# Kernel optimization log

Hardware: AMD Instinct MI355X
Metric: run time of the kernel (lower is better)

The kernel has to match this reference:

```python
import jax, jax.numpy as jnp
import numpy as np

N = 100000   # nodes
E = 1250000  # edges
IN, HID, OUT = 64, 128, 32


def _gcn_norm(edge_index, num_nodes):
    # add self loops, unit edge weights, symmetric normalization (PyG gcn_norm)
    loops = jnp.arange(num_nodes, dtype=edge_index.dtype)
    src = jnp.concatenate([edge_index[0], loops])
    dst = jnp.concatenate([edge_index[1], loops])
    w = jnp.ones(src.shape[0], dtype=jnp.float32)
    deg = jax.ops.segment_sum(w, dst, num_segments=num_nodes)  # degree at targets
    dis = jnp.where(deg > 0, jax.lax.rsqrt(deg), 0.0)
    norm = dis[src] * dis[dst]  # per-edge coefficient
    return src, dst, norm


def _gcn_conv(h, W, b, src, dst, norm, num_nodes):
    hw = h @ W                                 # [N, out] linear transform first
    msg = hw[src] * norm[:, None]              # gather + scale  [E+N, out]
    agg = jax.ops.segment_sum(msg, dst, num_segments=num_nodes)
    return agg + b


def setup_inputs() -> dict:
    key = jax.random.key(0)
    ks = jax.random.split(key, 8)
    x = jax.random.normal(ks[0], (N, IN), dtype=jnp.float32)
    edge_index = jax.random.randint(ks[1], (2, E), 0, N, dtype=jnp.int32)
    def glorot(k, fan_in, fan_out):
        s = np.sqrt(6.0 / (fan_in + fan_out)).astype(np.float32)
        return jax.random.uniform(k, (fan_in, fan_out), jnp.float32, -s, s)
    return {
        "x": x,
        "edge_index": edge_index,
        "W1": glorot(ks[2], IN, HID),   "b1": jnp.zeros((HID,), jnp.float32),
        "W_mu": glorot(ks[3], HID, OUT), "b_mu": jnp.zeros((OUT,), jnp.float32),
        "W_lv": glorot(ks[4], HID, OUT), "b_lv": jnp.zeros((OUT,), jnp.float32),
    }


def reference(x, edge_index, W1, b1, W_mu, b_mu, W_lv, b_lv):
    src, dst, norm = _gcn_norm(edge_index, N)
    h = _gcn_conv(x, W1, b1, src, dst, norm, N)
    h = jax.nn.selu(h)
    # dropout: eval mode (training=False) -> identity
    mu = _gcn_conv(h, W_mu, b_mu, src, dst, norm, N)
    logvar = _gcn_conv(h, W_lv, b_lv, src, dst, norm, N)
    return (mu, logvar)
```

## Files before the change

kernel.cpp:

```cpp
#include <hip/hip_runtime.h>
#include <math.h>

#define NN 100000
#define NE 1250000
#define DIN 64
#define DHID 128
#define DO2 64
#define DOUT 32

#define NBIN 256
#define BINW ((NN + NBIN - 1) / NBIN)
#define NSEG 153
#define C2 80
#define PADESRC 10944
#define P1_THREADS 1024
#define P1_EPT 8
#define P1_EPB (P1_THREADS * P1_EPT)

typedef unsigned int uint;
typedef unsigned short ushort;
typedef __attribute__((ext_vector_type(8))) short bf16x8;
typedef __attribute__((ext_vector_type(4))) float f32x4;

#define MFMA16(A, B, C) __builtin_amdgcn_mfma_f32_16x16x32_bf16(A, B, C, 0, 0, 0)

__device__ __forceinline__ ushort f2bf(float f) {
    uint u = __float_as_uint(f);
    uint r = (u + 0x7fffu + ((u >> 16) & 1u)) >> 16;
    return (ushort)r;
}
__device__ __forceinline__ uint pack2(float a, float b) {
    return (uint)f2bf(a) | ((uint)f2bf(b) << 16);
}
__device__ __forceinline__ float bflo(uint p) { return __uint_as_float(p << 16); }
__device__ __forceinline__ float bfhi(uint p) { return __uint_as_float(p & 0xffff0000u); }

__device__ __forceinline__ int nofk(int k) {
    return (k & 3) | (((k >> 3) & 3) << 2) | (((k >> 2) & 1) << 4) | ((k >> 5) << 5);
}

#define ACC8(A, P) do { \
    A##0 += bflo((P).x); A##1 += bfhi((P).x); \
    A##2 += bflo((P).y); A##3 += bfhi((P).y); \
    A##4 += bflo((P).z); A##5 += bfhi((P).z); \
    A##6 += bflo((P).w); A##7 += bfhi((P).w); } while (0)

__global__ __launch_bounds__(P1_THREADS) void scatter_direct(const int* __restrict__ src,
                                                             const int* __restrict__ dst,
                                                             uint* __restrict__ ebin,
                                                             int* __restrict__ cnt, int n) {
    __shared__ int hist[NBIN];
    int tid = threadIdx.x;
    if (tid < NBIN) hist[tid] = 0;
    __syncthreads();
    int bi = blockIdx.x;
    int base = bi * P1_EPB;
#pragma unroll
    for (int j = 0; j < P1_EPT; j++) {
        int i = base + j * P1_THREADS + tid;
        if (i < n) {
            int d = dst[i];
            int bb = d / BINW;
            uint e = ((uint)src[i] << 9) | (uint)(d - bb * BINW);
            int rk = atomicAdd(&hist[bb], 1);
            if (rk < C2) ebin[((size_t)bb * NSEG + bi) * C2 + rk] = e;
        }
    }
    __syncthreads();
    if (tid < NBIN) cnt[tid * NSEG + bi] = min(hist[tid], C2);
}

__global__ __launch_bounds__(512) void finalize_prep(const uint* __restrict__ ebin,
                                                     const int* __restrict__ cnt,
                                                     const float* __restrict__ x,
                                                     const float* __restrict__ W1,
                                                     const float* __restrict__ Wmu,
                                                     const float* __restrict__ Wlv,
                                                     float* __restrict__ dis,
                                                     int2* __restrict__ prange,
                                                     int* __restrict__ esrc,
                                                     uint* __restrict__ xb,
                                                     ushort* __restrict__ Wall) {
    __shared__ int hh[BINW];
    __shared__ int base_s[BINW];
    __shared__ int cur_s[BINW];
    __shared__ float dd[BINW];
    int b = blockIdx.x;
    int tid = threadIdx.x;
    int v0 = b * BINW;
    int nv = min(BINW, NN - v0);
    int pbase = PADESRC * b;
    for (int i = tid; i < BINW; i += 512) { hh[i] = 0; cur_s[i] = 0; }
    __syncthreads();
    int wv = tid >> 6, ln = tid & 63;
    for (int s = wv; s < NSEG; s += 8) {
        int m = cnt[b * NSEG + s];
        const uint* cell = ebin + ((size_t)b * NSEG + s) * C2;
        for (int j = ln; j < m; j += 64)
            atomicAdd(&hh[cell[j] & 511u], 1);
    }
    __syncthreads();
    int c = (tid < nv) ? hh[tid] : 0;
    int p = (c + 7) & ~7;
    __syncthreads();
    if (tid < nv) hh[tid] = p;
    __syncthreads();
    for (int off = 1; off < BINW; off <<= 1) {
        int t = (tid < nv && tid >= off) ? hh[tid - off] : 0;
        __syncthreads();
        if (tid < nv) hh[tid] += t;
        __syncthreads();
    }
    if (tid < nv) {
        int base = pbase + hh[tid] - p;
        base_s[tid] = base;
        prange[v0 + tid] = make_int2(base, base + p);
        float dv = rsqrtf((float)c + 1.0f);
        dis[v0 + tid] = dv;
        dd[tid] = dv;
        for (int j = c; j < p; j++) esrc[base + j] = NN;
    }
    __syncthreads();
    for (int s = wv; s < NSEG; s += 8) {
        int m = cnt[b * NSEG + s];
        const uint* cell = ebin + ((size_t)b * NSEG + s) * C2;
        for (int j = ln; j < m; j += 64) {
            uint e = cell[j];
            int l = (int)(e & 511u);
            int pos = base_s[l] + atomicAdd(&cur_s[l], 1);
            esrc[pos] = (int)(e >> 9);
        }
    }
    for (int idx = tid; idx < nv * 8; idx += 512) {
        int r = idx >> 3, q = idx & 7;
        float dv = dd[r];
        int row = v0 + r;
        const float4* xs = (const float4*)(x + (size_t)row * 64 + q * 8);
        float4 u0 = xs[0], u1 = xs[1];
        uint4 o;
        o.x = pack2(dv * u0.x, dv * u0.y);
        o.y = pack2(dv * u0.z, dv * u0.w);
        o.z = pack2(dv * u1.x, dv * u1.y);
        o.w = pack2(dv * u1.z, dv * u1.w);
        *(uint4*)(xb + (size_t)row * 32 + q * 4) = o;
    }
    if (b == NBIN - 1 && tid < 32) xb[(size_t)NN * 32 + tid] = 0;
    if (tid < 64) {
        int i = b * 64 + tid;
        if (i < 8192) {
            int lane = (i >> 3) & 63, e = i & 7;
            int fr = i >> 9;
            int t = fr >> 1, ks = fr & 1;
            int row = 16 * t + (lane & 15);
            int k = ks * 32 + (lane >> 4) * 8 + e;
            float w = W1[k * DHID + row];
            ushort hi = f2bf(w);
            Wall[i] = hi;
            Wall[8192 + i] = f2bf(w - bflo((uint)hi));
        } else {
            int ii = i - 8192;
            int lane = (ii >> 3) & 63, e = ii & 7;
            int fr = ii >> 9;
            int t2 = fr >> 2, ks = fr & 3;
            int nout = 16 * t2 + (lane & 15);
            int kpos = ks * 32 + (lane >> 4) * 8 + e;
            int h = nofk(kpos);
            float w = (nout < DOUT) ? Wmu[h * DOUT + nout] : Wlv[h * DOUT + (nout - DOUT)];
            ushort hi = f2bf(w);
            Wall[16384 + ii] = hi;
            Wall[24576 + ii] = f2bf(w - bflo((uint)hi));
        }
    }
}

#define GATHER_CORE(TBL)                                                            \
    int tid = threadIdx.x;                                                          \
    int lane = tid & 63;                                                            \
    int sub = lane & 15;                                                            \
    int epar = sub >> 3;                                                            \
    int f4 = (sub & 7) * 4;                                                         \
    int nlb = lane & 48;                                                            \
    int v = blockIdx.x * 16 + (tid >> 4);                 \
    int2 rng = prange[v];                                                           \
    int beg = rng.x, nb = rng.y - rng.x;                      \
    uint4 pv = *(const uint4*)(TBL + (size_t)v * 32 + f4);                          \
    float dv = dis[v];                                                              \
    int sreg  = esrc[beg + sub];                                                    \
    int sreg2 = esrc[beg + 16 + sub];                     \
    int svals[16];                                                                  \
    _Pragma("unroll")                                                               \
    for (int it = 0; it < 4; it++) {                                                \
        svals[2 * it]     = __shfl(sreg,  nlb | (epar + 4 * it));                   \
        svals[2 * it + 1] = __shfl(sreg,  nlb | (epar + 4 * it + 2));               \
    }                                                                               \
    _Pragma("unroll")                                                               \
    for (int it = 4; it < 8; it++) {                                                \
        svals[2 * it]     = __shfl(sreg2, nlb | (epar + 4 * it - 16));              \
        svals[2 * it + 1] = __shfl(sreg2, nlb | (epar + 4 * it - 14));              \
    }                                                                               \
    float a0 = 0.f, a1 = 0.f, a2 = 0.f, a3 = 0.f, a4 = 0.f, a5 = 0.f, a6 = 0.f, a7 = 0.f; \
    float b0 = 0.f, b1 = 0.f, b2 = 0.f, b3 = 0.f, b4 = 0.f, b5 = 0.f, b6 = 0.f, b7 = 0.f; \
    int lim = nb < 32 ? nb : 32;                                                    \
    int nit = lim >> 2;                                                             \
    _Pragma("unroll")                                                               \
    for (int it = 0; it < 4; it++) {                                                \
        int s0 = (it < nit) ? svals[2 * it]     : NN;                               \
        int s1 = (it < nit) ? svals[2 * it + 1] : NN;                               \
        uint4 pA = *(const uint4*)(TBL + (size_t)s0 * 32 + f4);                     \
        uint4 pB = *(const uint4*)(TBL + (size_t)s1 * 32 + f4);                     \
        ACC8(a, pA); ACC8(b, pB);                                                   \
    }                                                                               \
    if (__any(nit > 4)) {                                                           \
        _Pragma("unroll")                                                           \
        for (int it = 4; it < 8; it++) {                                            \
            int s0 = (it < nit) ? svals[2 * it]     : NN;                           \
            int s1 = (it < nit) ? svals[2 * it + 1] : NN;                           \
            uint4 pA = *(const uint4*)(TBL + (size_t)s0 * 32 + f4);                 \
            uint4 pB = *(const uint4*)(TBL + (size_t)s1 * 32 + f4);                 \
            ACC8(a, pA); ACC8(b, pB);                                               \
        }                                                                           \
    }                                                                               \
    if (__any(nb > 32)) {                                                           \
        for (int idx = 32 + epar; idx < nb; idx += 2) {      \
            int s = esrc[beg + idx];                                                \
            uint4 p = *(const uint4*)(TBL + (size_t)s * 32 + f4);                   \
            ACC8(b, p);                                                             \
        }                                                                           \
    }                                                                               \
    a0 += b0; a1 += b1; a2 += b2; a3 += b3; a4 += b4; a5 += b5; a6 += b6; a7 += b7; \
    a0 += __shfl_xor(a0, 8); a1 += __shfl_xor(a1, 8);                               \
    a2 += __shfl_xor(a2, 8); a3 += __shfl_xor(a3, 8);                               \
    a4 += __shfl_xor(a4, 8); a5 += __shfl_xor(a5, 8);                               \
    a6 += __shfl_xor(a6, 8); a7 += __shfl_xor(a7, 8);                               \
    ACC8(a, pv);

__global__ __launch_bounds__(256) void aggregateX(const uint* __restrict__ xsb,
                                                  const int2* __restrict__ prange,
                                                  const int* __restrict__ esrc,
                                                  const float* __restrict__ dis,
                                                  uint* __restrict__ axb) {
    GATHER_CORE(xsb)
    if (!epar) {
        uint4 o;
        o.x = pack2(dv * a0, dv * a1);
        o.y = pack2(dv * a2, dv * a3);
        o.z = pack2(dv * a4, dv * a5);
        o.w = pack2(dv * a6, dv * a7);
        *(uint4*)(axb + (size_t)v * 32 + f4) = o;
    }
}

__device__ __forceinline__ float selu_f(float v) {
    const float scale = 1.0507009873554805f;
    const float alpha = 1.6732632423543772f;
    return scale * (v > 0.f ? v : alpha * (expf(v) - 1.f));
}

__global__ __launch_bounds__(256) void gemm_fused(const uint* __restrict__ axb,
                                                  const ushort* __restrict__ Wall,
                                                  const float* __restrict__ b1,
                                                  const float* __restrict__ dis,
                                                  uint* __restrict__ hw2s) {
    __shared__ ushort Wlds[32768];
    int tid = threadIdx.x;
    int lane = tid & 63;
    int xr = lane & 15, q = lane >> 4;
    int rowbase = blockIdx.x * 128 + (tid >> 6) * 16;
    int v0 = rowbase + xr;
    int v1 = rowbase + 64 + xr;
    int v0c = min(v0, NN - 1);
    int v1c = min(v1, NN - 1);

    bf16x8 bf0[2], bf1[2];
#pragma unroll
    for (int ks = 0; ks < 2; ks++) {
        bf0[ks] = *(const bf16x8*)(axb + (size_t)v0c * 32 + ks * 16 + q * 4);
        bf1[ks] = *(const bf16x8*)(axb + (size_t)v1c * 32 + ks * 16 + q * 4);
    }

    {
        const uint4* wsrc = (const uint4*)Wall;
        uint4* wdst = (uint4*)Wlds;
#pragma unroll
        for (int c = 0; c < 16; c++) wdst[tid + c * 256] = wsrc[tid + c * 256];
    }
    __syncthreads();

    const char* ldsb = (const char*)Wlds;
    int lane16 = lane * 16;

    uint px0[8], py0[8], px1[8], py1[8];
#pragma unroll
    for (int t = 0; t < 8; t++) {
        bf16x8 ah0 = *(const bf16x8*)(ldsb + (t * 2 + 0) * 1024 + lane16);
        bf16x8 ah1 = *(const bf16x8*)(ldsb + (t * 2 + 1) * 1024 + lane16);
        bf16x8 al0 = *(const bf16x8*)(ldsb + 16384 + (t * 2 + 0) * 1024 + lane16);
        bf16x8 al1 = *(const bf16x8*)(ldsb + 16384 + (t * 2 + 1) * 1024 + lane16);
        f32x4 acc0 = {0.f, 0.f, 0.f, 0.f};
        f32x4 acc1 = {0.f, 0.f, 0.f, 0.f};
        acc0 = MFMA16(ah0, bf0[0], acc0); acc0 = MFMA16(al0, bf0[0], acc0);
        acc0 = MFMA16(ah1, bf0[1], acc0); acc0 = MFMA16(al1, bf0[1], acc0);
        acc1 = MFMA16(ah0, bf1[0], acc1); acc1 = MFMA16(al0, bf1[0], acc1);
        acc1 = MFMA16(ah1, bf1[1], acc1); acc1 = MFMA16(al1, bf1[1], acc1);
        float4 bb = *(const float4*)(b1 + 16 * t + 4 * q);
        px0[t] = pack2(selu_f(acc0[0] + bb.x), selu_f(acc0[1] + bb.y));
        py0[t] = pack2(selu_f(acc0[2] + bb.z), selu_f(acc0[3] + bb.w));
        px1[t] = pack2(selu_f(acc1[0] + bb.x), selu_f(acc1[1] + bb.y));
        py1[t] = pack2(selu_f(acc1[2] + bb.z), selu_f(acc1[3] + bb.w));
    }

    float dv0 = dis[v0c], dv1 = dis[v1c];
#pragma unroll
    for (int t2 = 0; t2 < 4; t2++) {
        f32x4 a0 = {0.f, 0.f, 0.f, 0.f};
        f32x4 a1 = {0.f, 0.f, 0.f, 0.f};
#pragma unroll
        for (int ks = 0; ks < 4; ks++) {
            bf16x8 ah = *(const bf16x8*)(ldsb + 32768 + (t2 * 4 + ks) * 1024 + lane16);
            bf16x8 al = *(const bf16x8*)(ldsb + 49152 + (t2 * 4 + ks) * 1024 + lane16);
            bf16x8 fr0, fr1;
            *(uint4*)&fr0 = make_uint4(px0[2 * ks], py0[2 * ks], px0[2 * ks + 1], py0[2 * ks + 1]);
            *(uint4*)&fr1 = make_uint4(px1[2 * ks], py1[2 * ks], px1[2 * ks + 1], py1[2 * ks + 1]);
            a0 = MFMA16(ah, fr0, a0); a0 = MFMA16(al, fr0, a0);
            a1 = MFMA16(ah, fr1, a1); a1 = MFMA16(al, fr1, a1);
        }
        if (v0 < NN) {
            uint2 pk;
            pk.x = pack2(dv0 * a0[0], dv0 * a0[1]);
            pk.y = pack2(dv0 * a0[2], dv0 * a0[3]);
            *(uint2*)(hw2s + (size_t)v0 * 32 + t2 * 8 + q * 2) = pk;
        }
        if (v1 < NN) {
            uint2 pk;
            pk.x = pack2(dv1 * a1[0], dv1 * a1[1]);
            pk.y = pack2(dv1 * a1[2], dv1 * a1[3]);
            *(uint2*)(hw2s + (size_t)v1 * 32 + t2 * 8 + q * 2) = pk;
        }
    }
}

__global__ __launch_bounds__(256) void aggregate2(const uint* __restrict__ hw2s,
                                                  const int2* __restrict__ prange,
                                                  const int* __restrict__ esrc,
                                                  const float* __restrict__ dis,
                                                  const float* __restrict__ bmu,
                                                  const float* __restrict__ blv,
                                                  float* __restrict__ out) {
    GATHER_CORE(hw2s)
    if (!epar) {
        int j = sub & 7;
        const float* bp = (j < 4) ? (bmu + 8 * j) : (blv + 8 * j - 32);
        float* op = (j < 4) ? (out + (size_t)v * DOUT + 8 * j)
                            : (out + (size_t)NN * DOUT + (size_t)v * DOUT + 8 * j - 32);
        float4 c0 = *(const float4*)bp;
        float4 c1 = *(const float4*)(bp + 4);
        *(float4*)op       = make_float4(dv * a0 + c0.x, dv * a1 + c0.y,
                                         dv * a2 + c0.z, dv * a3 + c0.w);
        *(float4*)(op + 4) = make_float4(dv * a4 + c1.x, dv * a5 + c1.y,
                                         dv * a6 + c1.z, dv * a7 + c1.w);
    }
}

extern "C" void kernel_launch(void* const* d_in, const int* in_sizes, int n_in,
                              void* d_out, int out_size, void* d_ws, size_t ws_size,
                              hipStream_t stream) {
    const float* x   = (const float*)d_in[0];
    const int*   ei  = (const int*)d_in[1];
    const int*   e_src = ei;
    const int*   e_dst = ei + NE;
    const float* W1  = (const float*)d_in[2];
    const float* b1  = (const float*)d_in[3];
    const float* Wmu = (const float*)d_in[4];
    const float* bmu = (const float*)d_in[5];
    const float* Wlv = (const float*)d_in[6];
    const float* blv = (const float*)d_in[7];
    float* out = (float*)d_out;

    char* ws = (char*)d_ws;
    size_t off = 0;
    auto alloc = [&](size_t bytes) -> void* {
        void* p = ws + off;
        off += (bytes + 255) & ~(size_t)255;
        return p;
    };
    int2*   prange    = (int2*)alloc((size_t)NN * 8);
    int*    esrc      = (int*)alloc(((size_t)NBIN * PADESRC + 64) * 4);
    int*    cnt       = (int*)alloc((size_t)NBIN * NSEG * 4);
    float*  dis       = (float*)alloc((size_t)NN * 4);
    ushort* Wall      = (ushort*)alloc((size_t)32768 * 2);
    uint*   xb        = (uint*)alloc((size_t)(NN + 1) * 32 * 4);
    uint*   axb       = (uint*)alloc((size_t)NN * 32 * 4);
    uint*   hw2s      = xb;
    uint*   ebin      = axb;

    scatter_direct<<<NSEG, P1_THREADS, 0, stream>>>(e_src, e_dst, ebin, cnt, NE);
    finalize_prep<<<NBIN, 512, 0, stream>>>(ebin, cnt, x, W1, Wmu, Wlv,
                                            dis, prange, esrc, xb, Wall);
    aggregateX<<<NN / 16, 256, 0, stream>>>(xb, prange, esrc, dis, axb);
    gemm_fused<<<(NN + 127) / 128, 256, 0, stream>>>(axb, Wall, b1, dis, hw2s);
    aggregate2<<<NN / 16, 256, 0, stream>>>(hw2s, prange, esrc, dis, bmu, blv, out);
}
```

Baseline: 203.0 us.

## Split node feature tables into four column planes to shrink gather footprint

Bf16 feature tables (xb, axb, hw2s) are stored as four column-plane arrays of 16 features per node instead of one 64-wide row. The gather kernels launch four times as many blocks, one plane per block group, with 8 edge lanes times 2 feature quarters per node. The aim is a smaller per-pass working set so random neighbor gathers hit cache better. In exchange, prange, esrc and neighbor indices are re-read four times, and the per-node reduction needs more shuffles.

```diff
diff --git a/kernel.cpp b/kernel.cpp
--- a/kernel.cpp
+++ b/kernel.cpp
@@ -16,6 +16,7 @@
 #define P1_THREADS 1024
 #define P1_EPT 8
 #define P1_EPB (P1_THREADS * P1_EPT)
+#define NVB 6250
 
 typedef unsigned int uint;
 typedef unsigned short ushort;
@@ -142,9 +143,10 @@
         o.y = pack2(dv * u0.z, dv * u0.w);
         o.z = pack2(dv * u1.x, dv * u1.y);
         o.w = pack2(dv * u1.z, dv * u1.w);
-        *(uint4*)(xb + (size_t)row * 32 + q * 4) = o;
-    }
-    if (b == NBIN - 1 && tid < 32) xb[(size_t)NN * 32 + tid] = 0;
+        *(uint4*)(xb + ((size_t)(q >> 1) * (NN + 1) + row) * 8 + (q & 1) * 4) = o;
+    }
+    if (b == NBIN - 1 && tid < 32)
+        xb[((size_t)(tid >> 3) * (NN + 1) + NN) * 8 + (tid & 7)] = 0;
     if (tid < 64) {
         int i = b * 64 + tid;
         if (i < 8192) {
@@ -173,65 +175,59 @@
     }
 }
 
-#define GATHER_CORE(TBL)                                                            \
+#define GATHER_CORE_P(TBL)                                                          \
     int tid = threadIdx.x;                                                          \
     int lane = tid & 63;                                                            \
     int sub = lane & 15;                                                            \
-    int epar = sub >> 3;                                                            \
-    int f4 = (sub & 7) * 4;                                                         \
+    int fl4 = (sub & 1) * 4;                                                        \
+    int es  = sub >> 1;                                                             \
     int nlb = lane & 48;                                                            \
-    int v = blockIdx.x * 16 + (tid >> 4);                 \
+    int pb = blockIdx.x / NVB;                                                      \
+    int vb = blockIdx.x - pb * NVB;                                                 \
+    int v = vb * 16 + (tid >> 4);                          \
+    const uint* tb = (TBL) + (size_t)pb * (NN + 1) * 8;                             \
     int2 rng = prange[v];                                                           \
     int beg = rng.x, nb = rng.y - rng.x;                      \
-    uint4 pv = *(const uint4*)(TBL + (size_t)v * 32 + f4);                          \
+    uint4 pv = *(const uint4*)(tb + (size_t)v * 8 + fl4);                           \
     float dv = dis[v];                                                              \
     int sreg  = esrc[beg + sub];                                                    \
     int sreg2 = esrc[beg + 16 + sub];                     \
-    int svals[16];                                                                  \
-    _Pragma("unroll")                                                               \
-    for (int it = 0; it < 4; it++) {                                                \
-        svals[2 * it]     = __shfl(sreg,  nlb | (epar + 4 * it));                   \
-        svals[2 * it + 1] = __shfl(sreg,  nlb | (epar + 4 * it + 2));               \
-    }                                                                               \
-    _Pragma("unroll")                                                               \
-    for (int it = 4; it < 8; it++) {                                                \
-        svals[2 * it]     = __shfl(sreg2, nlb | (epar + 4 * it - 16));              \
-        svals[2 * it + 1] = __shfl(sreg2, nlb | (epar + 4 * it - 14));              \
-    }                                                                               \
-    float a0 = 0.f, a1 = 0.f, a2 = 0.f, a3 = 0.f, a4 = 0.f, a5 = 0.f, a6 = 0.f, a7 = 0.f; \
-    float b0 = 0.f, b1 = 0.f, b2 = 0.f, b3 = 0.f, b4 = 0.f, b5 = 0.f, b6 = 0.f, b7 = 0.f; \
     int lim = nb < 32 ? nb : 32;                                                    \
-    int nit = lim >> 2;                                                             \
-    _Pragma("unroll")                                                               \
-    for (int it = 0; it < 4; it++) {                                                \
-        int s0 = (it < nit) ? svals[2 * it]     : NN;                               \
-        int s1 = (it < nit) ? svals[2 * it + 1] : NN;                               \
-        uint4 pA = *(const uint4*)(TBL + (size_t)s0 * 32 + f4);                     \
-        uint4 pB = *(const uint4*)(TBL + (size_t)s1 * 32 + f4);                     \
+    int sv0 = __shfl(sreg,  nlb | es);                                              \
+    int sv1 = __shfl(sreg,  nlb | (es + 8));                                        \
+    int sv2 = __shfl(sreg2, nlb | es);                                              \
+    int sv3 = __shfl(sreg2, nlb | (es + 8));                                        \
+    sv0 = (es      < lim) ? sv0 : NN;                                               \
+    sv1 = (es + 8  < lim) ? sv1 : NN;                                               \
+    sv2 = (es + 16 < lim) ? sv2 : NN;                                               \
+    sv3 = (es + 24 < lim) ? sv3 : NN;                                               \
+    float a0=0.f,a1=0.f,a2=0.f,a3=0.f,a4=0.f,a5=0.f,a6=0.f,a7=0.f;                  \
+    float b0=0.f,b1=0.f,b2=0.f,b3=0.f,b4=0.f,b5=0.f,b6=0.f,b7=0.f;                  \
+    {                                                                               \
+        uint4 pA = *(const uint4*)(tb + (size_t)sv0 * 8 + fl4);                     \
+        uint4 pB = *(const uint4*)(tb + (size_t)sv1 * 8 + fl4);                     \
         ACC8(a, pA); ACC8(b, pB);                                                   \
     }                                                                               \
-    if (__any(nit > 4)) {                                                           \
-        _Pragma("unroll")                                                           \
-        for (int it = 4; it < 8; it++) {                                            \
-            int s0 = (it < nit) ? svals[2 * it]     : NN;                           \
-            int s1 = (it < nit) ? svals[2 * it + 1] : NN;                           \
-            uint4 pA = *(const uint4*)(TBL + (size_t)s0 * 32 + f4);                 \
-            uint4 pB = *(const uint4*)(TBL + (size_t)s1 * 32 + f4);                 \
-            ACC8(a, pA); ACC8(b, pB);                                               \
-        }                                                                           \
+    if (__any(nb > 16)) {                                                           \
+        uint4 pA = *(const uint4*)(tb + (size_t)sv2 * 8 + fl4);                     \
+        uint4 pB = *(const uint4*)(tb + (size_t)sv3 * 8 + fl4);                     \
+        ACC8(a, pA); ACC8(b, pB);                                                   \
     }                                                                               \
     if (__any(nb > 32)) {                                                           \
-        for (int idx = 32 + epar; idx < nb; idx += 2) {      \
+        for (int idx = 32 + es; idx < nb; idx += 8) {        \
             int s = esrc[beg + idx];                                                \
-            uint4 p = *(const uint4*)(TBL + (size_t)s * 32 + f4);                   \
+            uint4 p = *(const uint4*)(tb + (size_t)s * 8 + fl4);                    \
             ACC8(b, p);                                                             \
         }                                                                           \
     }                                                                               \
     a0 += b0; a1 += b1; a2 += b2; a3 += b3; a4 += b4; a5 += b5; a6 += b6; a7 += b7; \
-    a0 += __shfl_xor(a0, 8); a1 += __shfl_xor(a1, 8);                               \
-    a2 += __shfl_xor(a2, 8); a3 += __shfl_xor(a3, 8);                               \
-    a4 += __shfl_xor(a4, 8); a5 += __shfl_xor(a5, 8);                               \
-    a6 += __shfl_xor(a6, 8); a7 += __shfl_xor(a7, 8);                               \
+    _Pragma("unroll")                                                               \
+    for (int m = 2; m <= 8; m <<= 1) {                                              \
+        a0 += __shfl_xor(a0, m); a1 += __shfl_xor(a1, m);                           \
+        a2 += __shfl_xor(a2, m); a3 += __shfl_xor(a3, m);                           \
+        a4 += __shfl_xor(a4, m); a5 += __shfl_xor(a5, m);                           \
+        a6 += __shfl_xor(a6, m); a7 += __shfl_xor(a7, m);                           \
+    }                                                                               \
     ACC8(a, pv);
 
 __global__ __launch_bounds__(256) void aggregateX(const uint* __restrict__ xsb,
@@ -239,14 +235,14 @@
                                                   const int* __restrict__ esrc,
                                                   const float* __restrict__ dis,
                                                   uint* __restrict__ axb) {
-    GATHER_CORE(xsb)
-    if (!epar) {
+    GATHER_CORE_P(xsb)
+    if (es == 0) {
         uint4 o;
         o.x = pack2(dv * a0, dv * a1);
         o.y = pack2(dv * a2, dv * a3);
         o.z = pack2(dv * a4, dv * a5);
         o.w = pack2(dv * a6, dv * a7);
-        *(uint4*)(axb + (size_t)v * 32 + f4) = o;
+        *(uint4*)(axb + ((size_t)pb * (NN + 1) + v) * 8 + fl4) = o;
     }
 }
 
@@ -274,8 +270,10 @@
     bf16x8 bf0[2], bf1[2];
 #pragma unroll
     for (int ks = 0; ks < 2; ks++) {
-        bf0[ks] = *(const bf16x8*)(axb + (size_t)v0c * 32 + ks * 16 + q * 4);
-        bf1[ks] = *(const bf16x8*)(axb + (size_t)v1c * 32 + ks * 16 + q * 4);
+        int qq = ks * 2 + (q >> 1);
+        int io = (q & 1) * 4;
+        bf0[ks] = *(const bf16x8*)(axb + ((size_t)qq * (NN + 1) + v0c) * 8 + io);
+        bf1[ks] = *(const bf16x8*)(axb + ((size_t)qq * (NN + 1) + v1c) * 8 + io);
     }
 
     {
@@ -328,13 +326,13 @@
             uint2 pk;
             pk.x = pack2(dv0 * a0[0], dv0 * a0[1]);
             pk.y = pack2(dv0 * a0[2], dv0 * a0[3]);
-            *(uint2*)(hw2s + (size_t)v0 * 32 + t2 * 8 + q * 2) = pk;
+            *(uint2*)(hw2s + ((size_t)t2 * (NN + 1) + v0) * 8 + q * 2) = pk;
         }
         if (v1 < NN) {
             uint2 pk;
             pk.x = pack2(dv1 * a1[0], dv1 * a1[1]);
             pk.y = pack2(dv1 * a1[2], dv1 * a1[3]);
-            *(uint2*)(hw2s + (size_t)v1 * 32 + t2 * 8 + q * 2) = pk;
+            *(uint2*)(hw2s + ((size_t)t2 * (NN + 1) + v1) * 8 + q * 2) = pk;
         }
     }
 }
@@ -346,12 +344,12 @@
                                                   const float* __restrict__ bmu,
                                                   const float* __restrict__ blv,
                                                   float* __restrict__ out) {
-    GATHER_CORE(hw2s)
-    if (!epar) {
-        int j = sub & 7;
-        const float* bp = (j < 4) ? (bmu + 8 * j) : (blv + 8 * j - 32);
-        float* op = (j < 4) ? (out + (size_t)v * DOUT + 8 * j)
-                            : (out + (size_t)NN * DOUT + (size_t)v * DOUT + 8 * j - 32);
+    GATHER_CORE_P(hw2s)
+    if (es == 0) {
+        int fl = fl4 >> 2;
+        int col = (pb & 1) * 16 + fl * 8;
+        const float* bp = (pb < 2) ? (bmu + col) : (blv + col);
+        float* op = out + (size_t)v * DOUT + col + ((pb < 2) ? 0 : (size_t)NN * DOUT);
         float4 c0 = *(const float4*)bp;
         float4 c1 = *(const float4*)(bp + 4);
         *(float4*)op       = make_float4(dv * a0 + c0.x, dv * a1 + c0.y,
@@ -389,14 +387,14 @@
     float*  dis       = (float*)alloc((size_t)NN * 4);
     ushort* Wall      = (ushort*)alloc((size_t)32768 * 2);
     uint*   xb        = (uint*)alloc((size_t)(NN + 1) * 32 * 4);
-    uint*   axb       = (uint*)alloc((size_t)NN * 32 * 4);
+    uint*   axb       = (uint*)alloc((size_t)(NN + 1) * 32 * 4);
     uint*   hw2s      = xb;
     uint*   ebin      = axb;
 
     scatter_direct<<<NSEG, P1_THREADS, 0, stream>>>(e_src, e_dst, ebin, cnt, NE);
     finalize_prep<<<NBIN, 512, 0, stream>>>(ebin, cnt, x, W1, Wmu, Wlv,
                                             dis, prange, esrc, xb, Wall);
-    aggregateX<<<NN / 16, 256, 0, stream>>>(xb, prange, esrc, dis, axb);
+    aggregateX<<<4 * NVB, 256, 0, stream>>>(xb, prange, esrc, dis, axb);
     gemm_fused<<<(NN + 127) / 128, 256, 0, stream>>>(axb, Wall, b1, dis, hw2s);
-    aggregate2<<<NN / 16, 256, 0, stream>>>(hw2s, prange, esrc, dis, bmu, blv, out);
-}
+    aggregate2<<<4 * NVB, 256, 0, stream>>>(hw2s, prange, esrc, dis, bmu, blv, out);
+}
```

After: 237.0 us. +16.7%, slower.
